# Kernel optimization log

Measured on AMD Instinct MI355X. Metric: run time of the kernel, lower is better.

## Reference

```python
import jax, jax.numpy as jnp
import numpy as np
from jax import lax

B = 512          # scoring batch size
NC = 10          # n_classes
N_LAB = 256      # int(B * plb), plb = 0.5 (labeled indices are the first N_LAB)
TOL = 1e-3       # gtg_t
MAX_ITER = 30    # gtg_i
INTERM = 128
CH = [64, 128, 256, 512]
SZ = [32, 16, 8, 4]
EMB = 512


def setup_inputs() -> dict:
    key = jax.random.key(0)
    ks = jax.random.split(key, 16)
    inp = {}
    for i, (c, s) in enumerate(zip(CH, SZ)):
        inp["feat%d" % i] = jax.random.normal(ks[i], (B, c, s, s), jnp.float32)
        inp["conv_w%d" % i] = jax.random.normal(ks[4 + i], (c, c, 3, 3), jnp.float32) * 0.05
        inp["conv_b%d" % i] = jnp.zeros((c,), jnp.float32)
        inp["bn_g%d" % i] = jnp.ones((c,), jnp.float32)
        inp["bn_b%d" % i] = jnp.zeros((c,), jnp.float32)
        inp["lin_w%d" % i] = jax.random.normal(ks[8 + i], (INTERM, c), jnp.float32) * 0.05
        inp["lin_b%d" % i] = jnp.zeros((INTERM,), jnp.float32)
    inp["fin_w"] = jax.random.normal(ks[12], (1, 4 * INTERM), jnp.float32) * 0.05
    inp["fin_b"] = jnp.zeros((1,), jnp.float32)
    inp["embedds"] = jax.random.normal(ks[13], (B, EMB), jnp.float32)
    inp["labels"] = jax.random.randint(ks[14], (B,), 0, NC)
    return inp


def _branch(x, cw, cb, g, b, lw, lb):
    # Conv3x3(same) -> BatchNorm (train mode, batch stats, eps=1e-5) -> ReLU -> GAP -> Linear -> ReLU
    y = lax.conv_general_dilated(x, cw, (1, 1), 'SAME',
                                 dimension_numbers=('NCHW', 'OIHW', 'NCHW')) + cb[None, :, None, None]
    m = y.mean(axis=(0, 2, 3), keepdims=True)
    v = ((y - m) ** 2).mean(axis=(0, 2, 3), keepdims=True)  # biased variance (train-mode BN)
    y = jax.nn.relu(g[None, :, None, None] * (y - m) * lax.rsqrt(v + 1e-5) + b[None, :, None, None])
    y = y.mean(axis=(2, 3))  # AvgPool2d(feature_size) == global average pool -> [B, C]
    return jax.nn.relu(y @ lw.T + lb)


def _gtg(E, labels):
    # get_A_e_d: pairwise euclidean distances clamped to [0.1, 1.0]
    sq = jnp.sum(E * E, axis=1)
    d2 = jnp.maximum(sq[:, None] + sq[None, :] - 2.0 * (E @ E.T), 0.0)
    A0 = jnp.clip(jnp.sqrt(d2), 0.1, 1.0)
    # rbf kernel: 7th nearest neighbor (ascending for 'e_d') gives per-sample sigma
    seventh = E[jnp.argsort(A0, axis=1)[:, 6]]
    sig = jnp.clip(jnp.sqrt(jnp.sum((E - seventh) ** 2, axis=1)), 0.1, 1.0)
    A = jnp.clip(jnp.exp(-(A0 ** 2) / (sig[:, None] * sig[None, :])), 0.0, 1.0)
    # threshold strategy 'mean' with AM_function == 'e_d': A = where(A > mean(A), 1, A)
    A = jnp.where(A > A.mean(), 1.0, A)
    # AM_strategy 'mixed' with 'e_d': flip only the labeled x labeled block
    A = A.at[:N_LAB, :N_LAB].set(1.0 - A[:N_LAB, :N_LAB])
    # get_X: one-hot for labeled (first N_LAB), uniform 1/NC for unlabeled
    X0 = jnp.concatenate([jax.nn.one_hot(labels[:N_LAB], NC, dtype=jnp.float32),
                          jnp.full((B - N_LAB, NC), 1.0 / NC, jnp.float32)], axis=0)
    hist0 = jnp.zeros((B, MAX_ITER), jnp.float32)

    def cond(c):
        return (c[3] > TOL) & (c[2] < MAX_ITER)

    def body(c):
        X, h, i, _ = c
        Xn = X * (A @ X)
        Xn = Xn / jnp.sum(Xn, axis=1, keepdims=True)
        ent = -jnp.sum(jnp.where(Xn > 0, Xn * jnp.log(Xn), 0.0), axis=1)
        h = lax.dynamic_update_slice(h, ent[:, None], (0, i))
        return (Xn, h, i + 1, jnp.linalg.norm(Xn - X))

    X, h, _, _ = lax.while_loop(cond, body, (X0, hist0, jnp.int32(0), jnp.float32(jnp.inf)))
    return h.mean(axis=1), X  # ent_strategy == 'mean'


def reference(feat0, feat1, feat2, feat3,
              conv_w0, conv_b0, bn_g0, bn_b0, lin_w0, lin_b0,
              conv_w1, conv_b1, bn_g1, bn_b1, lin_w1, lin_b1,
              conv_w2, conv_b2, bn_g2, bn_b2, lin_w2, lin_b2,
              conv_w3, conv_b3, bn_g3, bn_b3, lin_w3, lin_b3,
              fin_w, fin_b, embedds, labels):
    o0 = _branch(feat0, conv_w0, conv_b0, bn_g0, bn_b0, lin_w0, lin_b0)
    o1 = _branch(feat1, conv_w1, conv_b1, bn_g1, bn_b1, lin_w1, lin_b1)
    o2 = _branch(feat2, conv_w2, conv_b2, bn_g2, bn_b2, lin_w2, lin_b2)
    o3 = _branch(feat3, conv_w3, conv_b3, bn_g3, bn_b3, lin_w3, lin_b3)
    y_pred = (jnp.concatenate([o0, o1, o2, o3], axis=1) @ fin_w.T + fin_b)[:, 0]
    y_true, X = _gtg(embedds, labels)
    labeled_mask = jnp.arange(B) < N_LAB
    return (y_pred, y_true, X, labeled_mask)
```

## Files before the change

kernel.cpp:

```cpp
#include <hip/hip_runtime.h>
#include <hip/hip_bf16.h>
#include <math.h>

static constexpr int kNC = 10;
static constexpr int kNLab = 256;
static constexpr int kMaxIter = 30;

using short8 = __attribute__((ext_vector_type(8))) short;
using f32x4  = __attribute__((ext_vector_type(4))) float;

__device__ __forceinline__ unsigned short f2bf(float f) {
  unsigned int u = __float_as_uint(f);
  u += 0x7FFFu + ((u >> 16) & 1u);
  return (unsigned short)(u >> 16);
}
__device__ __forceinline__ float bf2f(unsigned short u) {
  return __uint_as_float(((unsigned int)u) << 16);
}

template <int C, int S>
__global__ __launch_bounds__(256) void xpack_kernel(const float* __restrict__ x,
                                                    unsigned short* __restrict__ xp) {
  __shared__ float t[C][S + 1];
  const int n = blockIdx.x / S, h = blockIdx.x % S;
  const float* src = x + (size_t)n * C * S * S;
  for (int e = threadIdx.x; e < C * S; e += 256) {
    int c = e / S, w = e % S;
    t[c][w] = src[((size_t)c * S + h) * S + w];
  }
  __syncthreads();
  unsigned short* dst = xp + ((size_t)(n * S + h) * S) * C;
  for (int e = threadIdx.x; e < C * S; e += 256) {
    int w = e / C, c = e % C;
    dst[(size_t)w * C + c] = f2bf(t[c][w]);
  }
}

__global__ void wpack_all(const float* __restrict__ w0, const float* __restrict__ w1,
                          const float* __restrict__ w2, const float* __restrict__ w3,
                          unsigned short* __restrict__ wpk) {
  int idx = blockIdx.x * 256 + threadIdx.x;
  if (idx >= 3133440) return;
  const float* w; int C, off;
  if (idx < 36864)        { w = w0; C = 64;  off = 0; }
  else if (idx < 184320)  { w = w1; C = 128; off = 36864; }
  else if (idx < 774144)  { w = w2; C = 256; off = 184320; }
  else                    { w = w3; C = 512; off = 774144; }
  int e = idx - off;
  int CO16T = C / 16, CIK = C / 32;
  int e8 = e & 7, l = (e >> 3) & 63;
  int rest = e >> 9;
  int co16 = rest % CO16T;
  int rest2 = rest / CO16T;
  int cik = rest2 % CIK, tap = rest2 / CIK;
  int co = co16 * 16 + (l & 15);
  int ci = cik * 32 + (l >> 4) * 8 + e8;
  wpk[idx] = f2bf(w[((size_t)co * C + ci) * 9 + tap]);
}

template <int C, int S, int NI, int NR, int WV, int BF, int MODE>
__global__ __launch_bounds__(WV * 64)
void conv_mfma(const unsigned short* __restrict__ xp, const unsigned short* __restrict__ wpk,
               const float* __restrict__ bias, unsigned short* __restrict__ y,
               float* __restrict__ psum, float* __restrict__ psq, int npart, int partBase,
               const float* __restrict__ scale, const float* __restrict__ shift,
               float* __restrict__ pp, int pxGlobalBase) {
  constexpr int SS = S * S;
  constexpr int PXB = NI * NR * S;
  constexpr int TPB = WV * 64;
  constexpr int HR = NR + 2, HC = S + 2;
  constexpr int CIK = C / 32, CO16T = C / 16;
  constexpr int UNITS = NI * HR * HC * 4;
  constexpr int NU = (UNITS + TPB - 1) / TPB;
  static_assert(WV * BF * 16 == PXB, "wave px mismatch");
  static_assert(MODE != 2 || BF == 4, "MODE2 assumes 64px/wave");
  __shared__ __align__(16) char xs[NI * HR * HC * 80];

  const int tid = threadIdx.x;
  const int wv = tid >> 6, l = tid & 63, l15 = l & 15, l4 = l >> 4;
  const int coblk = blockIdx.y;
  const int co_base = coblk * 64;
  const int pxb = blockIdx.x * PXB;
  const int n_t = pxb / SS;
  const int r0 = (pxb % SS) / S;

  int pxoff[BF];
#pragma unroll
  for (int bf = 0; bf < BF; ++bf) {
    int pxloc = wv * (BF * 16) + bf * 16 + l15;
    int ii = pxloc / (NR * S);
    int rr = (pxloc % (NR * S)) / S;
    int cc = pxloc % S;
    pxoff[bf] = ((ii * HR + rr) * HC + cc) * 80 + l4 * 16;
  }

  f32x4 acc[4][BF];
#pragma unroll
  for (int a = 0; a < 4; ++a)
#pragma unroll
    for (int b = 0; b < BF; ++b) acc[a][b] = (f32x4){0.f, 0.f, 0.f, 0.f};

  uint4 vreg[NU];
  auto loadU = [&](int cik) {
#pragma unroll
    for (int k = 0; k < NU; ++k) {
      int u = tid + k * TPB;
      uint4 v = {0u, 0u, 0u, 0u};
      if (u < UNITS) {
        int k16 = u & 3;
        int t = u >> 2;
        int hc = t % HC;
        int t2 = t / HC;
        int hr = t2 % HR;
        int ii = t2 / HR;
        int row = r0 + hr - 1, col = hc - 1;
        if (row >= 0 && row < S && col >= 0 && col < S)
          v = *(const uint4*)(xp + ((size_t)((n_t + ii) * S + row) * S + col) * C + cik * 32 + k16 * 8);
      }
      vreg[k] = v;
    }
  };

  loadU(0);
  for (int cik = 0; cik < CIK; ++cik) {
    __syncthreads();
#pragma unroll
    for (int k = 0; k < NU; ++k) {
      int u = tid + k * TPB;
      if (u < UNITS) *(uint4*)(xs + (u >> 2) * 80 + (u & 3) * 16) = vreg[k];
    }
    __syncthreads();
    if (cik + 1 < CIK) loadU(cik + 1);
#pragma unroll
    for (int tap = 0; tap < 9; ++tap) {
      const int tapoff = ((tap / 3) * HC + (tap % 3)) * 80;
      short8 wf[4], xf[BF];
#pragma unroll
      for (int af = 0; af < 4; ++af)
        wf[af] = *(const short8*)(wpk + ((size_t)((tap * CIK + cik) * CO16T + coblk * 4 + af) * 64 + l) * 8);
#pragma unroll
      for (int bf = 0; bf < BF; ++bf)
        xf[bf] = *(const short8*)(xs + pxoff[bf] + tapoff);
#pragma unroll
      for (int af = 0; af < 4; ++af)
#pragma unroll
        for (int bf = 0; bf < BF; ++bf)
          acc[af][bf] = __builtin_amdgcn_mfma_f32_16x16x32_bf16(wf[af], xf[bf], acc[af][bf], 0, 0, 0);
    }
  }

#pragma unroll
  for (int af = 0; af < 4; ++af) {
    const int co0 = co_base + af * 16 + l4 * 4;
    float4 bv = *(const float4*)(bias + co0);
    float s[4] = {0.f, 0.f, 0.f, 0.f}, q[4] = {0.f, 0.f, 0.f, 0.f};
    float4 sc4, sh4;
    if (MODE == 2) {
      sc4 = *(const float4*)(scale + co0);
      sh4 = *(const float4*)(shift + co0);
    }
#pragma unroll
    for (int bf = 0; bf < BF; ++bf) {
      float o[4];
#pragma unroll
      for (int r = 0; r < 4; ++r) o[r] = acc[af][bf][r] + ((const float*)&bv)[r];
      if (MODE == 0) {
        ushort4 pk;
        pk.x = f2bf(o[0]); pk.y = f2bf(o[1]); pk.z = f2bf(o[2]); pk.w = f2bf(o[3]);
        size_t px = (size_t)(pxb + wv * (BF * 16) + bf * 16 + l15);
        *(ushort4*)(y + px * C + co0) = pk;
      }
      if (MODE == 2) {
#pragma unroll
        for (int r = 0; r < 4; ++r)
          s[r] += fmaxf(fmaf(((const float*)&sc4)[r], o[r], ((const float*)&sh4)[r]), 0.f);
      } else {
#pragma unroll
        for (int r = 0; r < 4; ++r) { s[r] += o[r]; q[r] += o[r] * o[r]; }
      }
    }
#pragma unroll
    for (int m = 1; m < 16; m <<= 1) {
#pragma unroll
      for (int r = 0; r < 4; ++r) {
        s[r] += __shfl_xor(s[r], m);
        if (MODE != 2) q[r] += __shfl_xor(q[r], m);
      }
    }
    if (l15 == 0) {
      if (MODE == 2) {
        int n = (pxGlobalBase + pxb) / SS;
        int qw = ((pxGlobalBase + pxb) % SS) / 64 + wv;
#pragma unroll
        for (int r = 0; r < 4; ++r)
          pp[((size_t)(n * C + co0 + r)) * 16 + qw] = s[r];
      } else {
        int part = partBase + blockIdx.x * WV + wv;
#pragma unroll
        for (int r = 0; r < 4; ++r) {
          psum[(size_t)(co0 + r) * npart + part] = s[r];
          psq[(size_t)(co0 + r) * npart + part] = q[r];
        }
      }
    }
  }
}

__global__ __launch_bounds__(256)
void stats2_kernel(const float* __restrict__ psum, const float* __restrict__ psq,
                   const float* __restrict__ g, const float* __restrict__ bb,
                   float* __restrict__ scale, float* __restrict__ shift,
                   int npart, float invN) {
  int c = blockIdx.x;
  __shared__ float rs[256], rq[256];
  float s = 0.f, q = 0.f;
  for (int p = threadIdx.x; p < npart; p += 256) {
    s += psum[(size_t)c * npart + p];
    q += psq[(size_t)c * npart + p];
  }
  rs[threadIdx.x] = s; rq[threadIdx.x] = q;
  __syncthreads();
  for (int st = 128; st; st >>= 1) {
    if (threadIdx.x < st) { rs[threadIdx.x] += rs[threadIdx.x + st]; rq[threadIdx.x] += rq[threadIdx.x + st]; }
    __syncthreads();
  }
  if (threadIdx.x == 0) {
    float m = rs[0] * invN;
    float v = rq[0] * invN - m * m;
    float sc = g[c] / sqrtf(v + 1e-5f);
    scale[c] = sc;
    shift[c] = bb[c] - m * sc;
  }
}

template <int C, int S>
__global__ __launch_bounds__(256)
void pool_lin(const unsigned short* __restrict__ y, const float* __restrict__ scale,
              const float* __restrict__ shift, const float* __restrict__ lw,
              const float* __restrict__ lb, float* __restrict__ oc, int brOff) {
  constexpr int SS = S * S;
  int n = blockIdx.x;
  const unsigned short* yr = y + (size_t)n * SS * C;
  __shared__ float pl[C];
  if (C >= 256) {
    for (int co = threadIdx.x; co < C; co += 256) {
      float sc = scale[co], sh = shift[co], s = 0.f;
      for (int p = 0; p < SS; ++p) s += fmaxf(fmaf(sc, bf2f(yr[(size_t)p * C + co]), sh), 0.f);
      pl[co] = s * (1.f / SS);
    }
  } else {
    constexpr int G = 256 / C;
    int co = threadIdx.x % C;
    int sl = threadIdx.x / C;
    float sc = scale[co], sh = shift[co], s = 0.f;
    for (int p = sl; p < SS; p += G) s += fmaxf(fmaf(sc, bf2f(yr[(size_t)p * C + co]), sh), 0.f);
    __shared__ float red[256];
    red[threadIdx.x] = s;
    __syncthreads();
    if (threadIdx.x < C) {
      float t = 0.f;
      for (int gg = 0; gg < G; ++gg) t += red[gg * C + co];
      pl[co] = t * (1.f / SS);
    }
  }
  __syncthreads();
  if (threadIdx.x < 128) {
    int j = threadIdx.x;
    const float* wr = lw + (size_t)j * C;
    float s = 0.f;
    for (int t = 0; t < C; ++t) s = fmaf(pl[t], wr[t], s);
    s += lb[j];
    oc[n * 512 + brOff + j] = fmaxf(s, 0.f);
  }
}

__global__ void poolfin_kernel(const float* __restrict__ pp, float* __restrict__ pooled) {
  int i = blockIdx.x * 256 + threadIdx.x;
  if (i >= 512 * 64) return;
  float s = 0.f;
  for (int qn = 0; qn < 16; ++qn) s += pp[(size_t)i * 16 + qn];
  pooled[i] = s * (1.f / 1024.f);
}

__global__ void lin_kernel(const float* __restrict__ pooled, const float* __restrict__ lw,
                           const float* __restrict__ lb, float* __restrict__ oc,
                           int C, int brOff) {
  int idx = blockIdx.x * 256 + threadIdx.x;
  if (idx >= 512 * 128) return;
  int j = idx & 127, n = idx >> 7;
  const float4* pr = (const float4*)(pooled + (size_t)n * C);
  const float4* wr = (const float4*)(lw + (size_t)j * C);
  float s = 0.f;
  for (int t = 0; t < C / 4; ++t) {
    float4 a = pr[t], b = wr[t];
    s += a.x * b.x + a.y * b.y + a.z * b.z + a.w * b.w;
  }
  s += lb[j];
  oc[n * 512 + brOff + j] = fmaxf(s, 0.f);
}

__global__ void ypred_kernel(const float* __restrict__ oc, const float* __restrict__ fw,
                             const float* __restrict__ fb, float* __restrict__ out) {
  int wv = threadIdx.x >> 6, l = threadIdx.x & 63;
  int n = blockIdx.x * 4 + wv;
  float s = 0.f;
  for (int k = l; k < 512; k += 64) s += oc[n * 512 + k] * fw[k];
#pragma unroll
  for (int m = 32; m; m >>= 1) s += __shfl_down(s, m);
  if (l == 0) out[n] = s + fb[0];
}

__global__ void sqnorm_kernel(const float* __restrict__ E, float* __restrict__ sq) {
  int wv = threadIdx.x >> 6, l = threadIdx.x & 63;
  int n = blockIdx.x * 4 + wv;
  const float* row = E + (size_t)n * 512;
  float s = 0.f;
  for (int k = l; k < 512; k += 64) { float v = row[k]; s += v * v; }
#pragma unroll
  for (int m = 32; m; m >>= 1) s += __shfl_down(s, m);
  if (l == 0) sq[n] = s;
}

__global__ __launch_bounds__(256) void a0_kernel(const float* __restrict__ E,
                                                 const float* __restrict__ sq,
                                                 float* __restrict__ A0) {
  int bi = blockIdx.x / 32, bj = blockIdx.x % 32;
  int ti = threadIdx.x % 16, tj = threadIdx.x / 16;
  __shared__ float Ei[16][68], Ej[16][68];
  float acc = 0.f;
  for (int k0 = 0; k0 < 512; k0 += 64) {
    for (int e = threadIdx.x; e < 1024; e += 256) {
      int rr = e >> 6, cc = e & 63;
      Ei[rr][cc] = E[(size_t)(bi * 16 + rr) * 512 + k0 + cc];
      Ej[rr][cc] = E[(size_t)(bj * 16 + rr) * 512 + k0 + cc];
    }
    __syncthreads();
#pragma unroll 16
    for (int kk = 0; kk < 64; ++kk) acc = fmaf(Ei[tj][kk], Ej[ti][kk], acc);
    __syncthreads();
  }
  int i = bi * 16 + tj, j = bj * 16 + ti;
  float d2 = fmaxf(sq[i] + sq[j] - 2.f * acc, 0.f);
  A0[(size_t)i * 512 + j] = fminf(fmaxf(sqrtf(d2), 0.1f), 1.0f);
}

__global__ void seventh_kernel(const float* __restrict__ A0, int* __restrict__ idx7) {
  int i = blockIdx.x * 256 + threadIdx.x;
  if (i >= 512) return;
  float v[7]; int ix[7];
#pragma unroll
  for (int t = 0; t < 7; ++t) { v[t] = 3.4e38f; ix[t] = 0; }
  const float* row = A0 + (size_t)i * 512;
  for (int j = 0; j < 512; ++j) {
    float a = row[j];
    if (a < v[6]) {
      int pos = 6;
      while (pos > 0 && a < v[pos - 1]) { v[pos] = v[pos - 1]; ix[pos] = ix[pos - 1]; --pos; }
      v[pos] = a; ix[pos] = j;
    }
  }
  idx7[i] = ix[6];
}

__global__ void sig_kernel(const float* __restrict__ E, const int* __restrict__ idx7,
                           float* __restrict__ sig) {
  int wv = threadIdx.x >> 6, l = threadIdx.x & 63;
  int n = blockIdx.x * 4 + wv;
  const float* r1 = E + (size_t)n * 512;
  const float* r2 = E + (size_t)idx7[n] * 512;
  float s = 0.f;
  for (int k = l; k < 512; k += 64) { float d = r1[k] - r2[k]; s += d * d; }
#pragma unroll
  for (int m = 32; m; m >>= 1) s += __shfl_down(s, m);
  if (l == 0) sig[n] = fminf(fmaxf(sqrtf(s), 0.1f), 1.0f);
}

__global__ void aexp_kernel(const float* __restrict__ A0, const float* __restrict__ sig,
                            float* __restrict__ A, float* __restrict__ part) {
  int t = blockIdx.x * 256 + threadIdx.x;
  int base = t * 4;
  int i = base >> 9, j0 = base & 511;
  float si = sig[i];
  float4 a = *(const float4*)(A0 + base);
  float4 o;
  o.x = fminf(fmaxf(expf(-a.x * a.x / (si * sig[j0 + 0])), 0.f), 1.f);
  o.y = fminf(fmaxf(expf(-a.y * a.y / (si * sig[j0 + 1])), 0.f), 1.f);
  o.z = fminf(fmaxf(expf(-a.z * a.z / (si * sig[j0 + 2])), 0.f), 1.f);
  o.w = fminf(fmaxf(expf(-a.w * a.w / (si * sig[j0 + 3])), 0.f), 1.f);
  *(float4*)(A + base) = o;
  float lsum = o.x + o.y + o.z + o.w;
#pragma unroll
  for (int m = 32; m; m >>= 1) lsum += __shfl_down(lsum, m);
  __shared__ float sred[4];
  if ((threadIdx.x & 63) == 0) sred[threadIdx.x >> 6] = lsum;
  __syncthreads();
  if (threadIdx.x == 0) part[blockIdx.x] = sred[0] + sred[1] + sred[2] + sred[3];
}

__global__ void meanred_kernel(const float* __restrict__ part, float* __restrict__ meanA) {
  if (threadIdx.x == 0 && blockIdx.x == 0) {
    float s = 0.f;
    for (int p = 0; p < 256; ++p) s += part[p];
    meanA[0] = s * (1.0f / 262144.0f);
  }
}

__global__ void thresh_kernel(float* __restrict__ A, const float* __restrict__ meanA) {
  int t = blockIdx.x * 256 + threadIdx.x;
  int base = t * 4;
  int i = base >> 9, j0 = base & 511;
  float m = meanA[0];
  float4 v = *(const float4*)(A + base);
  v.x = v.x > m ? 1.f : v.x;
  v.y = v.y > m ? 1.f : v.y;
  v.z = v.z > m ? 1.f : v.z;
  v.w = v.w > m ? 1.f : v.w;
  if (i < kNLab && j0 < kNLab) {
    v.x = 1.f - v.x; v.y = 1.f - v.y; v.z = 1.f - v.z; v.w = 1.f - v.w;
  }
  *(float4*)(A + base) = v;
}

__global__ __launch_bounds__(1024, 4)
void gtg2(const float* __restrict__ A, const int* __restrict__ labels,
          float* __restrict__ out) {
  const int tid = threadIdx.x;
  const int w = tid >> 6, l = tid & 63;
  const int r = l & 15, g = l >> 4;
  const int i = w * 16 + r;
  __shared__ float Xs[2][256][12];
  __shared__ float dredw[2][16];
  __shared__ int labs[256];

  if (tid < 256) labs[tid] = labels[tid];
  for (int e = tid; e < 256 * 12; e += 1024)
    (&Xs[0][0][0])[e] = ((e % 12) < 10) ? 0.1f : 0.f;
  __syncthreads();

  const float* Ar = A + (size_t)(256 + i) * 512 + g * 64;
  float areg[64];
#pragma unroll
  for (int q = 0; q < 16; ++q) {
    float4 v = *(const float4*)(Ar + 256 + q * 4);
    areg[q * 4 + 0] = v.x; areg[q * 4 + 1] = v.y;
    areg[q * 4 + 2] = v.z; areg[q * 4 + 3] = v.w;
  }
  float lp[10];
#pragma unroll
  for (int c = 0; c < 10; ++c) lp[c] = 0.f;
#pragma unroll
  for (int q = 0; q < 16; ++q) {
    float4 v = *(const float4*)(Ar + q * 4);
    float av[4] = {v.x, v.y, v.z, v.w};
#pragma unroll
    for (int k = 0; k < 4; ++k) {
      int lab = labs[g * 64 + q * 4 + k];
#pragma unroll
      for (int c = 0; c < 10; ++c) lp[c] += (lab == c) ? av[k] : 0.f;
    }
  }

  float entsum = 0.f;
  float nrm2 = 1e30f;
  int cur = 0;
  for (int it = 0; it < kMaxIter; ++it) {
    if (it > 0 && sqrtf(nrm2) <= 0.001f) break;
    float ax[10];
#pragma unroll
    for (int c = 0; c < 10; ++c) ax[c] = lp[c];
#pragma unroll
    for (int jj = 0; jj < 64; ++jj) {
      const float* xr = &Xs[cur][g * 64 + jj][0];
      float4 x0 = *(const float4*)(xr);
      float4 x1 = *(const float4*)(xr + 4);
      float2 x2 = *(const float2*)(xr + 8);
      float a = areg[jj];
      ax[0] = fmaf(a, x0.x, ax[0]); ax[1] = fmaf(a, x0.y, ax[1]);
      ax[2] = fmaf(a, x0.z, ax[2]); ax[3] = fmaf(a, x0.w, ax[3]);
      ax[4] = fmaf(a, x1.x, ax[4]); ax[5] = fmaf(a, x1.y, ax[5]);
      ax[6] = fmaf(a, x1.z, ax[6]); ax[7] = fmaf(a, x1.w, ax[7]);
      ax[8] = fmaf(a, x2.x, ax[8]); ax[9] = fmaf(a, x2.y, ax[9]);
    }
#pragma unroll
    for (int c = 0; c < 10; ++c) {
      ax[c] += __shfl_xor(ax[c], 16);
      ax[c] += __shfl_xor(ax[c], 32);
    }
    float dp = 0.f;
    if (g == 0) {
      float xn[10], ssum = 0.f;
#pragma unroll
      for (int c = 0; c < 10; ++c) { xn[c] = Xs[cur][i][c] * ax[c]; ssum += xn[c]; }
      float ent = 0.f;
#pragma unroll
      for (int c = 0; c < 10; ++c) {
        float xv = xn[c] / ssum;
        if (xv > 0.f) ent -= xv * logf(xv);
        float d = xv - Xs[cur][i][c];
        dp += d * d;
        Xs[cur ^ 1][i][c] = xv;
      }
      entsum += ent;
    }
#pragma unroll
    for (int m = 1; m < 64; m <<= 1) dp += __shfl_xor(dp, m);
    if (l == 0) dredw[it & 1][w] = dp;
    __syncthreads();
    float s = 0.f;
#pragma unroll
    for (int q = 0; q < 16; ++q) s += dredw[it & 1][q];
    nrm2 = s;
    cur ^= 1;
  }

  if (g == 0) out[512 + 256 + i] = entsum * (1.0f / 30.0f);
  for (int e = tid; e < 256; e += 1024) {
    out[512 + e] = 0.f;
    out[6144 + e] = 1.f;
    out[6144 + 256 + e] = 0.f;
  }
  for (int e = tid; e < 2560; e += 1024) {
    int rr = e / 10, c = e % 10;
    out[1024 + e] = (labs[rr] == c) ? 1.f : 0.f;
    out[1024 + 2560 + e] = Xs[cur][rr][c];
  }
}

extern "C" void kernel_launch(void* const* d_in, const int* in_sizes, int n_in,
                              void* d_out, int out_size, void* d_ws, size_t ws_size,
                              hipStream_t stream) {
  (void)in_sizes; (void)n_in; (void)out_size;

  const float* feat[4]; const float* cw[4]; const float* cbp[4];
  const float* bg[4]; const float* bbp[4]; const float* lw[4]; const float* lbp[4];
  for (int b = 0; b < 4; ++b) {
    int base = b * 7;
    feat[b] = (const float*)d_in[base + 0];
    cw[b]  = (const float*)d_in[base + 1];
    cbp[b] = (const float*)d_in[base + 2];
    bg[b]  = (const float*)d_in[base + 3];
    bbp[b] = (const float*)d_in[base + 4];
    lw[b]  = (const float*)d_in[base + 5];
    lbp[b] = (const float*)d_in[base + 6];
  }
  const float* finw = (const float*)d_in[28];
  const float* finb = (const float*)d_in[29];
  const float* emb  = (const float*)d_in[30];
  const int* labels = (const int*)d_in[31];
  float* out = (float*)d_out;

  float* wsf = (float*)d_ws;
  unsigned short* xpad = (unsigned short*)wsf;
  unsigned short* yP   = (unsigned short*)(wsf + 4194304);
  unsigned short* wpk  = (unsigned short*)(wsf + 12582912);
  size_t off = 14149632;
  float* psum = wsf + off; off += 524288;
  float* psq  = wsf + off; off += 524288;
  float* pp   = wsf + off; off += 524288;
  float* scale = wsf + off; off += 512;
  float* shift = wsf + off; off += 512;
  float* pooled = wsf + off; off += 491520;
  float* oc = wsf + off; off += 262144;
  float* sq = wsf + off; off += 512;
  float* A0 = wsf + off; off += 262144;
  float* Am = wsf + off; off += 262144;
  float* sig = wsf + off; off += 512;
  int* idx7 = (int*)(wsf + off); off += 512;
  float* meanPart = wsf + off; off += 256;
  float* meanA = wsf + off; off += 4;
  size_t yb0_off = off;
  unsigned short* yB0 = (unsigned short*)(wsf + yb0_off);
  const bool bigB0 = ws_size >= (yb0_off + 16777216) * sizeof(float);

  unsigned short* wpkB[4] = {wpk, wpk + 36864, wpk + 184320, wpk + 774144};

  wpack_all<<<(3133440 + 255) / 256, 256, 0, stream>>>(cw[0], cw[1], cw[2], cw[3], wpk);

  for (int c = 0; c < 2; ++c) {
    xpack_kernel<128, 16><<<256 * 16, 256, 0, stream>>>(feat[1] + (size_t)c * 8388608, xpad);
    conv_mfma<128, 16, 1, 8, 4, 2, 0><<<dim3(512, 2), 256, 0, stream>>>(
        xpad, wpkB[1], cbp[1], yP + (size_t)c * 8388608, psum, psq, 4096, c * 2048,
        nullptr, nullptr, nullptr, 0);
  }
  stats2_kernel<<<128, 256, 0, stream>>>(psum, psq, bg[1], bbp[1], scale, shift, 4096, 1.f / 131072.f);
  pool_lin<128, 16><<<512, 256, 0, stream>>>(yP, scale, shift, lw[1], lbp[1], oc, 128);

  xpack_kernel<256, 8><<<512 * 8, 256, 0, stream>>>(feat[2], xpad);
  conv_mfma<256, 8, 2, 8, 4, 2, 0><<<dim3(256, 4), 256, 0, stream>>>(
      xpad, wpkB[2], cbp[2], yP, psum, psq, 1024, 0, nullptr, nullptr, nullptr, 0);
  stats2_kernel<<<256, 256, 0, stream>>>(psum, psq, bg[2], bbp[2], scale, shift, 1024, 1.f / 32768.f);
  pool_lin<256, 8><<<512, 256, 0, stream>>>(yP, scale, shift, lw[2], lbp[2], oc, 256);

  xpack_kernel<512, 4><<<512 * 4, 256, 0, stream>>>(feat[3], xpad);
  conv_mfma<512, 4, 8, 4, 4, 2, 0><<<dim3(64, 8), 256, 0, stream>>>(
      xpad, wpkB[3], cbp[3], yP, psum, psq, 256, 0, nullptr, nullptr, nullptr, 0);
  stats2_kernel<<<512, 256, 0, stream>>>(psum, psq, bg[3], bbp[3], scale, shift, 256, 1.f / 8192.f);
  pool_lin<512, 4><<<512, 256, 0, stream>>>(yP, scale, shift, lw[3], lbp[3], oc, 384);

  if (bigB0) {
    for (int c = 0; c < 4; ++c) {
      xpack_kernel<64, 32><<<128 * 32, 256, 0, stream>>>(feat[0] + (size_t)c * 8388608, xpad);
      conv_mfma<64, 32, 1, 8, 4, 4, 0><<<dim3(512, 1), 256, 0, stream>>>(
          xpad, wpkB[0], cbp[0], yB0 + (size_t)c * 8388608, psum, psq, 8192, c * 2048,
          nullptr, nullptr, nullptr, 0);
    }
    stats2_kernel<<<64, 256, 0, stream>>>(psum, psq, bg[0], bbp[0], scale, shift, 8192, 1.f / 524288.f);
    pool_lin<64, 32><<<512, 256, 0, stream>>>(yB0, scale, shift, lw[0], lbp[0], oc, 0);
  } else {
    for (int c = 0; c < 4; ++c) {
      xpack_kernel<64, 32><<<128 * 32, 256, 0, stream>>>(feat[0] + (size_t)c * 8388608, xpad);
      conv_mfma<64, 32, 1, 8, 4, 4, 1><<<dim3(512, 1), 256, 0, stream>>>(
          xpad, wpkB[0], cbp[0], nullptr, psum, psq, 8192, c * 2048, nullptr, nullptr, nullptr, 0);
    }
    stats2_kernel<<<64, 256, 0, stream>>>(psum, psq, bg[0], bbp[0], scale, shift, 8192, 1.f / 524288.f);
    for (int c = 0; c < 4; ++c) {
      xpack_kernel<64, 32><<<128 * 32, 256, 0, stream>>>(feat[0] + (size_t)c * 8388608, xpad);
      conv_mfma<64, 32, 1, 8, 4, 4, 2><<<dim3(512, 1), 256, 0, stream>>>(
          xpad, wpkB[0], cbp[0], nullptr, nullptr, nullptr, 0, 0, scale, shift, pp, c * 131072);
    }
    poolfin_kernel<<<128, 256, 0, stream>>>(pp, pooled);
    lin_kernel<<<256, 256, 0, stream>>>(pooled, lw[0], lbp[0], oc, 64, 0);
  }

  ypred_kernel<<<128, 256, 0, stream>>>(oc, finw, finb, out);
  sqnorm_kernel<<<128, 256, 0, stream>>>(emb, sq);
  a0_kernel<<<1024, 256, 0, stream>>>(emb, sq, A0);
  seventh_kernel<<<2, 256, 0, stream>>>(A0, idx7);
  sig_kernel<<<128, 256, 0, stream>>>(emb, idx7, sig);
  aexp_kernel<<<256, 256, 0, stream>>>(A0, sig, Am, meanPart);
  meanred_kernel<<<1, 64, 0, stream>>>(meanPart, meanA);
  thresh_kernel<<<256, 256, 0, stream>>>(Am, meanA);

  gtg2<<<1, 1024, 0, stream>>>(Am, labels, out);
}
```

Before: 997.5 us.

## Pre-pack GTG affinity block for coalesced loads and pad shared X rows

```diff
diff --git a/kernel.cpp b/kernel.cpp
--- a/kernel.cpp
+++ b/kernel.cpp
@@ -421,36 +421,51 @@
   *(float4*)(A + base) = v;
 }
 
-__global__ __launch_bounds__(1024, 4)
-void gtg2(const float* __restrict__ A, const int* __restrict__ labels,
-          float* __restrict__ out) {
+__global__ void apack_kernel(const float* __restrict__ A, float* __restrict__ Apk) {
+  int t = blockIdx.x * 256 + threadIdx.x;
+  if (t >= 16384) return;
+  int q = t >> 10, tid = t & 1023;
+  int w = tid >> 6, l = tid & 63;
+  int i = w * 16 + (l & 15), g = l >> 4;
+  float4 v = *(const float4*)(A + (size_t)(256 + i) * 512 + 256 + g * 64 + q * 4);
+  *(float4*)(Apk + (size_t)t * 4) = v;
+}
+
+__global__ __launch_bounds__(1024) __attribute__((amdgpu_waves_per_eu(4, 4)))
+void gtg3(const float* __restrict__ Apk, const float* __restrict__ A,
+          const int* __restrict__ labels, float* __restrict__ out) {
   const int tid = threadIdx.x;
   const int w = tid >> 6, l = tid & 63;
   const int r = l & 15, g = l >> 4;
   const int i = w * 16 + r;
-  __shared__ float Xs[2][256][12];
+  __shared__ __align__(16) float Xs[2][3088];
   __shared__ float dredw[2][16];
   __shared__ int labs[256];
 
   if (tid < 256) labs[tid] = labels[tid];
-  for (int e = tid; e < 256 * 12; e += 1024)
-    (&Xs[0][0][0])[e] = ((e % 12) < 10) ? 0.1f : 0.f;
+  for (int e = tid; e < 3088; e += 1024) {
+    int o = e % 772;
+    Xs[0][e] = (o < 768 && (o % 12) < 10) ? 0.1f : 0.f;
+  }
   __syncthreads();
 
-  const float* Ar = A + (size_t)(256 + i) * 512 + g * 64;
   float areg[64];
 #pragma unroll
   for (int q = 0; q < 16; ++q) {
-    float4 v = *(const float4*)(Ar + 256 + q * 4);
+    float4 v = *(const float4*)(Apk + ((size_t)q * 1024 + tid) * 4);
     areg[q * 4 + 0] = v.x; areg[q * 4 + 1] = v.y;
     areg[q * 4 + 2] = v.z; areg[q * 4 + 3] = v.w;
   }
+#pragma unroll
+  for (int k = 0; k < 64; ++k) asm volatile("" : "+v"(areg[k]));
+
+  const float* Arl = A + (size_t)(256 + i) * 512 + g * 64;
   float lp[10];
 #pragma unroll
   for (int c = 0; c < 10; ++c) lp[c] = 0.f;
 #pragma unroll
   for (int q = 0; q < 16; ++q) {
-    float4 v = *(const float4*)(Ar + q * 4);
+    float4 v = *(const float4*)(Arl + q * 4);
     float av[4] = {v.x, v.y, v.z, v.w};
 #pragma unroll
     for (int k = 0; k < 4; ++k) {
@@ -459,18 +474,23 @@
       for (int c = 0; c < 10; ++c) lp[c] += (lab == c) ? av[k] : 0.f;
     }
   }
+#pragma unroll
+  for (int c = 0; c < 10; ++c) asm volatile("" : "+v"(lp[c]));
+
+  const int irow = (i >> 6) * 772 + (i & 63) * 12;
 
   float entsum = 0.f;
   float nrm2 = 1e30f;
   int cur = 0;
   for (int it = 0; it < kMaxIter; ++it) {
     if (it > 0 && sqrtf(nrm2) <= 0.001f) break;
+    const float* Xc = &Xs[cur][0];
     float ax[10];
 #pragma unroll
     for (int c = 0; c < 10; ++c) ax[c] = lp[c];
 #pragma unroll
     for (int jj = 0; jj < 64; ++jj) {
-      const float* xr = &Xs[cur][g * 64 + jj][0];
+      const float* xr = Xc + g * 772 + jj * 12;
       float4 x0 = *(const float4*)(xr);
       float4 x1 = *(const float4*)(xr + 4);
       float2 x2 = *(const float2*)(xr + 8);
@@ -488,17 +508,19 @@
     }
     float dp = 0.f;
     if (g == 0) {
+      const float* xo = Xc + irow;
+      float* xn_p = &Xs[cur ^ 1][irow];
       float xn[10], ssum = 0.f;
 #pragma unroll
-      for (int c = 0; c < 10; ++c) { xn[c] = Xs[cur][i][c] * ax[c]; ssum += xn[c]; }
+      for (int c = 0; c < 10; ++c) { xn[c] = xo[c] * ax[c]; ssum += xn[c]; }
       float ent = 0.f;
 #pragma unroll
       for (int c = 0; c < 10; ++c) {
         float xv = xn[c] / ssum;
         if (xv > 0.f) ent -= xv * logf(xv);
-        float d = xv - Xs[cur][i][c];
+        float d = xv - xo[c];
         dp += d * d;
-        Xs[cur ^ 1][i][c] = xv;
+        xn_p[c] = xv;
       }
       entsum += ent;
     }
@@ -522,7 +544,7 @@
   for (int e = tid; e < 2560; e += 1024) {
     int rr = e / 10, c = e % 10;
     out[1024 + e] = (labs[rr] == c) ? 1.f : 0.f;
-    out[1024 + 2560 + e] = Xs[cur][rr][c];
+    out[1024 + 2560 + e] = Xs[cur][(rr >> 6) * 772 + (rr & 63) * 12 + c];
   }
 }
 
@@ -568,6 +590,7 @@
   int* idx7 = (int*)(wsf + off); off += 512;
   float* meanPart = wsf + off; off += 256;
   float* meanA = wsf + off; off += 4;
+  float* Apk = wsf + off; off += 65536;
   size_t yb0_off = off;
   unsigned short* yB0 = (unsigned short*)(wsf + yb0_off);
   const bool bigB0 = ws_size >= (yb0_off + 16777216) * sizeof(float);
@@ -631,5 +654,6 @@
   meanred_kernel<<<1, 64, 0, stream>>>(meanPart, meanA);
   thresh_kernel<<<256, 256, 0, stream>>>(Am, meanA);
 
-  gtg2<<<1, 1024, 0, stream>>>(Am, labels, out);
-}
+  apack_kernel<<<64, 256, 0, stream>>>(Am, Apk);
+  gtg3<<<1, 1024, 0, stream>>>(Apk, Am, labels, out);
+}
```

New measurement: 990.3 us. About the same (-0.7%).
